# Optimization experiments

Measured on AMD Instinct MI355X. Metric: run time of the kernel, lower is better.

Reference implementation:

```python
import jax, jax.numpy as jnp
import numpy as np

N_IN, N_OUT, BATCH, LEVELS = 8192, 256, 1024, 2


def binarize(x):
    # clip + sign with straight-through gradient (Ioffe trick)
    c = jnp.clip(x, -1.0, 1.0)
    return c + jax.lax.stop_gradient(jnp.sign(c) - c)


def setup_inputs() -> dict:
    key = jax.random.key(0)
    ks = jax.random.split(key, 5)
    stdv = 1.0 / np.sqrt(N_IN)
    x = jax.random.normal(ks[0], (LEVELS, BATCH, N_IN), dtype=jnp.float32)
    w = jax.random.normal(ks[1], (32, N_IN, N_OUT), dtype=jnp.float32) * stdv
    gamma = jnp.ones((1,), dtype=jnp.float32)
    rand_map_0 = jax.random.randint(ks[2], (N_IN,), 0, N_IN, dtype=jnp.int32)
    rand_map_1 = jax.random.randint(ks[3], (N_IN,), 0, N_IN, dtype=jnp.int32)
    rand_map_2 = jax.random.randint(ks[4], (N_IN,), 0, N_IN, dtype=jnp.int32)
    pruning_mask = jnp.ones((N_IN, N_OUT), dtype=jnp.float32)
    return {"x": x, "w": w, "gamma": gamma, "pruning_mask": pruning_mask,
            "rand_map_0": rand_map_0, "rand_map_1": rand_map_1, "rand_map_2": rand_map_2}


def reference(x, w, gamma, pruning_mask, rand_map_0, rand_map_1, rand_map_2):
    # levels==2, LUT==True, BINARY==True path of binary_dense
    constraint_gamma = jnp.abs(gamma[0])
    cw = constraint_gamma * binarize(w)            # [32, n_in, n_out]
    mw = cw * pruning_mask[None, :, :]             # pruned clamped weights
    B, n_out = x.shape[1], mw.shape[2]
    out = jnp.zeros((B, n_out), dtype=x.dtype)
    for l in range(LEVELS):
        xl = x[l]                                   # [B, n_in] residual-binarization level l
        # original input + three random-map gathered shuffles
        streams = [xl, xl[:, rand_map_0], xl[:, rand_map_1], xl[:, rand_map_2]]
        # pos = (1+sign)/2*|x|, neg = (1-sign)/2*|x|  (one-hot sign selectors scaled by magnitude)
        pos = [(1.0 + binarize(s)) * 0.5 * jnp.abs(s) for s in streams]
        neg = [(1.0 - binarize(s)) * 0.5 * jnp.abs(s) for s in streams]
        for c in range(16):                         # truth table over 4 binary inputs
            bits = [(c >> (3 - i)) & 1 for i in range(4)]  # x is MSB, xs2 is LSB; 0->pos, 1->neg
            f = pos[0] if bits[0] == 0 else neg[0]
            for i in range(1, 4):
                f = f * (pos[i] if bits[i] == 0 else neg[i])
            out = out + f @ mw[16 * l + c]
    return out
```

## Files before the change

kernel.cpp:

```cpp
#include <hip/hip_runtime.h>
#include <hip/hip_fp16.h>


#define N_IN   8192
#define N_OUT  256
#define BATCH  1024
#define LEVELS 2

#define KSLICES 64
#define BTILES  4
#define BT      256
#define CHUNK_K 8
#define ROWP    264

__global__ __launch_bounds__(256) void pass_mc(const float* __restrict__ x,
                                               const int* __restrict__ rm0,
                                               const int* __restrict__ rm1,
                                               const int* __restrict__ rm2,
                                               unsigned int* __restrict__ mc) {
  __shared__ float xrow[N_IN];
  const int lb = blockIdx.x;
  const size_t base = (size_t)lb * N_IN;
  const float4* xv = (const float4*)(x + base);
  const int t = threadIdx.x;
#pragma unroll
  for (int j = 0; j < 8; ++j) {
    float4 v = xv[t + j * 256];
    *(float4*)&xrow[4 * (t + j * 256)] = v;
  }
  __syncthreads();
#pragma unroll 4
  for (int j = 0; j < 32; ++j) {
    const int k = t + j * 256;
    const int r0 = rm0[k], r1 = rm1[k], r2 = rm2[k];
    const float s0 = xrow[k], s1 = xrow[r0], s2 = xrow[r1], s3 = xrow[r2];
    const float m = fabsf(s0 * s1 * s2 * s3);
    const unsigned c = ((s0 < 0.f) ? 8u : 0u) | ((s1 < 0.f) ? 4u : 0u) |
                       ((s2 < 0.f) ? 2u : 0u) | ((s3 < 0.f) ? 1u : 0u);
    mc[base + k] = (__float_as_uint(m) & ~0xFu) | c;
  }
}

__global__ __launch_bounds__(512, 2) void main_fma(const float* __restrict__ w,
                                                   const float* __restrict__ mask,
                                                   const unsigned int* __restrict__ mc,
                                                   float* __restrict__ part) {
  __shared__ __half lw[4 * 16 * ROWP];
  __shared__ unsigned int lmc[LEVELS * CHUNK_K * 256];

  const int ks = blockIdx.x;
  const int bt = blockIdx.y;
  const int t = threadIdx.x;
  const int lane = t & 63;
  const int wid = t >> 6;
  const int wb = wid * 32;

  float acc[32][4];
#pragma unroll
  for (int i = 0; i < 32; ++i) {
    acc[i][0] = 0.f; acc[i][1] = 0.f; acc[i][2] = 0.f; acc[i][3] = 0.f;
  }

  const int s_ku = t >> 7;
  const int s_r  = (t >> 3) & 15;
  const int s_ob = (t & 7) * 32;

  for (int kc = 0; kc < 128 / CHUNK_K; ++kc) {
    const int k0 = ks * 128 + kc * CHUNK_K;
    __syncthreads();
    {
      const int l = t >> 8, b = t & 255;
      const unsigned int* src =
          mc + ((size_t)(l * BATCH + bt * BT + b) * N_IN + k0);
      const uint4 v0 = *(const uint4*)src;
      const uint4 v1 = *(const uint4*)(src + 4);
      unsigned int* dst = &lmc[l * (CHUNK_K * 256) + b];
      dst[0 * 256] = v0.x; dst[1 * 256] = v0.y; dst[2 * 256] = v0.z; dst[3 * 256] = v0.w;
      dst[4 * 256] = v1.x; dst[5 * 256] = v1.y; dst[6 * 256] = v1.z; dst[7 * 256] = v1.w;
    }
    __syncthreads();

    for (int sub = 0; sub < 4; ++sub) {
      if (sub) __syncthreads();
      {
        const int u = sub * 4 + s_ku;
        const int l = u >> 3, kk = u & 7;
        const int k = k0 + kk;
        const int row = l * 16 + s_r;
        const float* wsrc = w + ((size_t)(row * N_IN + k) * N_OUT + s_ob);
        const float* msrc = mask + ((size_t)k * N_OUT + s_ob);
        __half hbuf[32];
#pragma unroll
        for (int j = 0; j < 8; ++j) {
          const float4 wv = *(const float4*)(wsrc + j * 4);
          const float4 mv = *(const float4*)(msrc + j * 4);
          hbuf[4 * j + 0] = __float2half((wv.x > 0.f) ? mv.x : ((wv.x < 0.f) ? -mv.x : 0.f));
          hbuf[4 * j + 1] = __float2half((wv.y > 0.f) ? mv.y : ((wv.y < 0.f) ? -mv.y : 0.f));
          hbuf[4 * j + 2] = __float2half((wv.z > 0.f) ? mv.z : ((wv.z < 0.f) ? -mv.z : 0.f));
          hbuf[4 * j + 3] = __float2half((wv.w > 0.f) ? mv.w : ((wv.w < 0.f) ? -mv.w : 0.f));
        }
        __half* dst = &lw[s_ku * (16 * ROWP) + s_r * ROWP + s_ob];
#pragma unroll
        for (int j = 0; j < 4; ++j) *(uint4*)(dst + j * 8) = *(const uint4*)&hbuf[j * 8];
      }
      __syncthreads();

#pragma unroll
      for (int ul = 0; ul < 4; ++ul) {
        const int u = sub * 4 + ul;
        const int l = u >> 3, kk = u & 7;
        const unsigned int* mrow = &lmc[l * (CHUNK_K * 256) + kk * 256 + wb];
        const __half* wbase = &lw[ul * (16 * ROWP)];
#pragma unroll
        for (int i = 0; i < 32; i += 4) {
          const uint4 q = *(const uint4*)(mrow + i);
#define DO_B(UQ, AI)                                                        \
  {                                                                         \
    const unsigned uq = (UQ);                                               \
    const float m = __uint_as_float(uq & ~0xFu);                            \
    union { uint2 u2; __half2 h[2]; } wv_;                                  \
    wv_.u2 = *(const uint2*)(wbase + (uq & 0xFu) * ROWP + lane * 4);        \
    acc[AI][0] += m * __half2float(wv_.h[0].x);                             \
    acc[AI][1] += m * __half2float(wv_.h[0].y);                             \
    acc[AI][2] += m * __half2float(wv_.h[1].x);                             \
    acc[AI][3] += m * __half2float(wv_.h[1].y);                             \
  }
          DO_B(q.x, i + 0)
          DO_B(q.y, i + 1)
          DO_B(q.z, i + 2)
          DO_B(q.w, i + 3)
#undef DO_B
        }
      }
    }
  }

  float* dst = part + ((size_t)(ks * BATCH + bt * BT + wb) * N_OUT) + lane * 4;
#pragma unroll
  for (int i = 0; i < 32; ++i) *(float4*)(dst + (size_t)i * N_OUT) = *(const float4*)acc[i];
}

__global__ __launch_bounds__(256) void reduce_part(const float* __restrict__ part,
                                                   const float* __restrict__ gamma,
                                                   float* __restrict__ out) {
  const int b = blockIdx.x, o = threadIdx.x;
  const float g = fabsf(gamma[0]);
  const float* p = part + (size_t)b * N_OUT + o;
  float s = 0.f;
#pragma unroll
  for (int ks = 0; ks < KSLICES; ++ks) s += p[(size_t)ks * BATCH * N_OUT];
  out[b * N_OUT + o] = g * s;
}

extern "C" void kernel_launch(void* const* d_in, const int* in_sizes, int n_in,
                              void* d_out, int out_size, void* d_ws, size_t ws_size,
                              hipStream_t stream) {
  const float* x     = (const float*)d_in[0];
  const float* w     = (const float*)d_in[1];
  const float* gamma = (const float*)d_in[2];
  const float* mask  = (const float*)d_in[3];
  const int* rm0     = (const int*)d_in[4];
  const int* rm1     = (const int*)d_in[5];
  const int* rm2     = (const int*)d_in[6];
  float* out = (float*)d_out;

  unsigned int* mc = (unsigned int*)d_ws;
  float* part = (float*)((char*)d_ws + (size_t)LEVELS * BATCH * N_IN * 4);
  (void)in_sizes; (void)n_in; (void)out_size; (void)ws_size;

  pass_mc<<<dim3(LEVELS * BATCH), 256, 0, stream>>>(x, rm0, rm1, rm2, mc);
  main_fma<<<dim3(KSLICES, BTILES), 512, 0, stream>>>(w, mask, mc, part);
  reduce_part<<<dim3(BATCH), 256, 0, stream>>>(part, gamma, out);
}
```

Baseline: 1.020 ms.

## Prepack weights to 8-bit half-high bytes and atomically reduce into output

Adds a pre-pass that converts sign(w)*mask into one byte per weight (the high byte of the fp16 value), so main_fma streams a quarter of the weight bytes and expands them with byte-perm instructions. The batch tile is halved to 128 with 4 blocks per CU, which doubles the blocks and lowers register pressure but makes each block re-read the weights for fewer batch rows. The partial buffer and its reduction kernel are replaced by float atomicAdd into a zeroed output, followed by a gamma-scaling kernel. In exchange the packing pass reads the full fp32 weight tensor on every call, and the atomics make the summation order nondeterministic.

```diff
diff --git a/kernel.cpp b/kernel.cpp
--- a/kernel.cpp
+++ b/kernel.cpp
@@ -8,10 +8,38 @@
 #define LEVELS 2
 
 #define KSLICES 64
-#define BTILES  4
-#define BT      256
-#define CHUNK_K 8
-#define ROWP    264
+#define BTILES  8
+#define BT      128
+
+__global__ __launch_bounds__(256) void zero_out(float* __restrict__ out) {
+  out[blockIdx.x * 256 + threadIdx.x] = 0.f;
+}
+
+__global__ __launch_bounds__(256) void scale_out(float* __restrict__ out,
+                                                 const float* __restrict__ gamma) {
+  const int i = blockIdx.x * 256 + threadIdx.x;
+  out[i] *= fabsf(gamma[0]);
+}
+
+__global__ __launch_bounds__(256) void pass_w(const float* __restrict__ w,
+                                              const float* __restrict__ mask,
+                                              unsigned char* __restrict__ sw) {
+  const size_t base = ((size_t)blockIdx.x * 256 + threadIdx.x) * 8;
+  const size_t mo = base & (size_t)(N_IN * N_OUT - 1);
+  float wv[8], mv[8];
+  *(float4*)&wv[0] = *(const float4*)(w + base);
+  *(float4*)&wv[4] = *(const float4*)(w + base + 4);
+  *(float4*)&mv[0] = *(const float4*)(mask + mo);
+  *(float4*)&mv[4] = *(const float4*)(mask + mo + 4);
+  unsigned int u0 = 0, u1 = 0;
+#pragma unroll
+  for (int j = 0; j < 8; ++j) {
+    const float v = (wv[j] > 0.f) ? mv[j] : ((wv[j] < 0.f) ? -mv[j] : 0.f);
+    const unsigned int b = (unsigned int)(__half_as_ushort(__float2half(v)) >> 8);
+    if (j < 4) u0 |= b << (j * 8); else u1 |= b << ((j - 4) * 8);
+  }
+  *(uint2*)(sw + base) = make_uint2(u0, u1);
+}
 
 __global__ __launch_bounds__(256) void pass_mc(const float* __restrict__ x,
                                                const int* __restrict__ rm0,
@@ -41,89 +69,81 @@
   }
 }
 
-__global__ __launch_bounds__(512, 2) void main_fma(const float* __restrict__ w,
-                                                   const float* __restrict__ mask,
+__global__ __launch_bounds__(512, 4) void main_fma(const unsigned char* __restrict__ sw,
                                                    const unsigned int* __restrict__ mc,
-                                                   float* __restrict__ part) {
-  __shared__ __half lw[4 * 16 * ROWP];
-  __shared__ unsigned int lmc[LEVELS * CHUNK_K * 256];
+                                                   float* __restrict__ out) {
+  __shared__ __half lw[4 * 16 * 256];
+  __shared__ unsigned int lmc[16 * 128];
 
   const int ks = blockIdx.x;
   const int bt = blockIdx.y;
   const int t = threadIdx.x;
   const int lane = t & 63;
   const int wid = t >> 6;
-  const int wb = wid * 32;
+  const int wb = wid * 16;
 
-  float acc[32][4];
+  float acc[16][4];
 #pragma unroll
-  for (int i = 0; i < 32; ++i) {
-    acc[i][0] = 0.f; acc[i][1] = 0.f; acc[i][2] = 0.f; acc[i][3] = 0.f;
-  }
+  for (int i = 0; i < 16; ++i) { acc[i][0] = acc[i][1] = acc[i][2] = acc[i][3] = 0.f; }
 
-  const int s_ku = t >> 7;
-  const int s_r  = (t >> 3) & 15;
-  const int s_ob = (t & 7) * 32;
+  const int s_kul = t >> 7;
+  const int s_r   = (t >> 3) & 15;
+  const int s_ob  = (t & 7) * 32;
 
-  for (int kc = 0; kc < 128 / CHUNK_K; ++kc) {
-    const int k0 = ks * 128 + kc * CHUNK_K;
+  const int g_l = t >> 8;
+  const int g_b = (t >> 1) & 127;
+  const int g_h = t & 1;
+
+  for (int kc = 0; kc < 16; ++kc) {
+    const int k0 = ks * 128 + kc * 8;
     __syncthreads();
     {
-      const int l = t >> 8, b = t & 255;
-      const unsigned int* src =
-          mc + ((size_t)(l * BATCH + bt * BT + b) * N_IN + k0);
-      const uint4 v0 = *(const uint4*)src;
-      const uint4 v1 = *(const uint4*)(src + 4);
-      unsigned int* dst = &lmc[l * (CHUNK_K * 256) + b];
-      dst[0 * 256] = v0.x; dst[1 * 256] = v0.y; dst[2 * 256] = v0.z; dst[3 * 256] = v0.w;
-      dst[4 * 256] = v1.x; dst[5 * 256] = v1.y; dst[6 * 256] = v1.z; dst[7 * 256] = v1.w;
+      const uint4 v = *(const uint4*)(mc + ((size_t)(g_l * BATCH + bt * BT + g_b) * N_IN + k0 + g_h * 4));
+      unsigned int* dst = &lmc[(g_l * 8 + g_h * 4) * 128 + g_b];
+      dst[0 * 128] = v.x; dst[1 * 128] = v.y; dst[2 * 128] = v.z; dst[3 * 128] = v.w;
     }
     __syncthreads();
 
     for (int sub = 0; sub < 4; ++sub) {
       if (sub) __syncthreads();
       {
-        const int u = sub * 4 + s_ku;
-        const int l = u >> 3, kk = u & 7;
-        const int k = k0 + kk;
-        const int row = l * 16 + s_r;
-        const float* wsrc = w + ((size_t)(row * N_IN + k) * N_OUT + s_ob);
-        const float* msrc = mask + ((size_t)k * N_OUT + s_ob);
-        __half hbuf[32];
+        const int ku = sub * 4 + s_kul;
+        const int l = ku >> 3, kk = ku & 7;
+        const unsigned char* src =
+            sw + ((size_t)((l * 16 + s_r) * N_IN + (k0 + kk)) * N_OUT + s_ob);
+        const uint4 a = ((const uint4*)src)[0];
+        const uint4 b = ((const uint4*)src)[1];
+        unsigned int dec[16];
+        const unsigned int xs[8] = {a.x, a.y, a.z, a.w, b.x, b.y, b.z, b.w};
 #pragma unroll
         for (int j = 0; j < 8; ++j) {
-          const float4 wv = *(const float4*)(wsrc + j * 4);
-          const float4 mv = *(const float4*)(msrc + j * 4);
-          hbuf[4 * j + 0] = __float2half((wv.x > 0.f) ? mv.x : ((wv.x < 0.f) ? -mv.x : 0.f));
-          hbuf[4 * j + 1] = __float2half((wv.y > 0.f) ? mv.y : ((wv.y < 0.f) ? -mv.y : 0.f));
-          hbuf[4 * j + 2] = __float2half((wv.z > 0.f) ? mv.z : ((wv.z < 0.f) ? -mv.z : 0.f));
-          hbuf[4 * j + 3] = __float2half((wv.w > 0.f) ? mv.w : ((wv.w < 0.f) ? -mv.w : 0.f));
+          dec[2 * j + 0] = __builtin_amdgcn_perm(0u, xs[j], 0x01040004u);
+          dec[2 * j + 1] = __builtin_amdgcn_perm(0u, xs[j], 0x03040204u);
         }
-        __half* dst = &lw[s_ku * (16 * ROWP) + s_r * ROWP + s_ob];
+        unsigned int* dst = (unsigned int*)&lw[(s_kul * 16 + s_r) * 256 + s_ob];
 #pragma unroll
-        for (int j = 0; j < 4; ++j) *(uint4*)(dst + j * 8) = *(const uint4*)&hbuf[j * 8];
+        for (int j = 0; j < 4; ++j) *(uint4*)(dst + 4 * j) = *(const uint4*)&dec[4 * j];
       }
       __syncthreads();
 
 #pragma unroll
-      for (int ul = 0; ul < 4; ++ul) {
-        const int u = sub * 4 + ul;
-        const int l = u >> 3, kk = u & 7;
-        const unsigned int* mrow = &lmc[l * (CHUNK_K * 256) + kk * 256 + wb];
-        const __half* wbase = &lw[ul * (16 * ROWP)];
+      for (int kul = 0; kul < 4; ++kul) {
+        const int ku = sub * 4 + kul;
+        const unsigned int* mrow = &lmc[ku * 128 + wb];
+        const __half* wsel = lw + kul * 4096 + lane * 4;
 #pragma unroll
-        for (int i = 0; i < 32; i += 4) {
+        for (int i = 0; i < 16; i += 4) {
           const uint4 q = *(const uint4*)(mrow + i);
-#define DO_B(UQ, AI)                                                        \
-  {                                                                         \
-    const unsigned uq = (UQ);                                               \
-    const float m = __uint_as_float(uq & ~0xFu);                            \
-    union { uint2 u2; __half2 h[2]; } wv_;                                  \
-    wv_.u2 = *(const uint2*)(wbase + (uq & 0xFu) * ROWP + lane * 4);        \
-    acc[AI][0] += m * __half2float(wv_.h[0].x);                             \
-    acc[AI][1] += m * __half2float(wv_.h[0].y);                             \
-    acc[AI][2] += m * __half2float(wv_.h[1].x);                             \
-    acc[AI][3] += m * __half2float(wv_.h[1].y);                             \
+#define DO_B(UQ, AI)                                                      \
+  {                                                                       \
+    const unsigned uq = (UQ);                                             \
+    const float m = __uint_as_float(uq & 0xFFFFFFF0u);                    \
+    union { uint2 u; __half h[4]; } wv_;                                  \
+    wv_.u = *(const uint2*)(wsel + ((uq & 15u) << 8));                    \
+    acc[AI][0] = fmaf(m, __half2float(wv_.h[0]), acc[AI][0]);             \
+    acc[AI][1] = fmaf(m, __half2float(wv_.h[1]), acc[AI][1]);             \
+    acc[AI][2] = fmaf(m, __half2float(wv_.h[2]), acc[AI][2]);             \
+    acc[AI][3] = fmaf(m, __half2float(wv_.h[3]), acc[AI][3]);             \
   }
           DO_B(q.x, i + 0)
           DO_B(q.y, i + 1)
@@ -135,21 +155,15 @@
     }
   }
 
-  float* dst = part + ((size_t)(ks * BATCH + bt * BT + wb) * N_OUT) + lane * 4;
+  float* dst0 = out + (size_t)(bt * BT + wb) * N_OUT + lane * 4;
 #pragma unroll
-  for (int i = 0; i < 32; ++i) *(float4*)(dst + (size_t)i * N_OUT) = *(const float4*)acc[i];
-}
-
-__global__ __launch_bounds__(256) void reduce_part(const float* __restrict__ part,
-                                                   const float* __restrict__ gamma,
-                                                   float* __restrict__ out) {
-  const int b = blockIdx.x, o = threadIdx.x;
-  const float g = fabsf(gamma[0]);
-  const float* p = part + (size_t)b * N_OUT + o;
-  float s = 0.f;
-#pragma unroll
-  for (int ks = 0; ks < KSLICES; ++ks) s += p[(size_t)ks * BATCH * N_OUT];
-  out[b * N_OUT + o] = g * s;
+  for (int i = 0; i < 16; ++i) {
+    float* d = dst0 + (size_t)i * N_OUT;
+    atomicAdd(d + 0, acc[i][0]);
+    atomicAdd(d + 1, acc[i][1]);
+    atomicAdd(d + 2, acc[i][2]);
+    atomicAdd(d + 3, acc[i][3]);
+  }
 }
 
 extern "C" void kernel_launch(void* const* d_in, const int* in_sizes, int n_in,
@@ -165,10 +179,12 @@
   float* out = (float*)d_out;
 
   unsigned int* mc = (unsigned int*)d_ws;
-  float* part = (float*)((char*)d_ws + (size_t)LEVELS * BATCH * N_IN * 4);
+  unsigned char* sw = (unsigned char*)d_ws + (size_t)LEVELS * BATCH * N_IN * 4;
   (void)in_sizes; (void)n_in; (void)out_size; (void)ws_size;
 
+  zero_out<<<dim3(BATCH), 256, 0, stream>>>(out);
+  pass_w<<<dim3(32 * N_IN * N_OUT / (256 * 8)), 256, 0, stream>>>(w, mask, sw);
   pass_mc<<<dim3(LEVELS * BATCH), 256, 0, stream>>>(x, rm0, rm1, rm2, mc);
-  main_fma<<<dim3(KSLICES, BTILES), 512, 0, stream>>>(w, mask, mc, part);
-  reduce_part<<<dim3(BATCH), 256, 0, stream>>>(part, gamma, out);
+  main_fma<<<dim3(KSLICES, BTILES), 512, 0, stream>>>(sw, mc, out);
+  scale_out<<<dim3(BATCH), 256, 0, stream>>>(out, gamma);
 }
```

Result: no change. 1.037 ms (+1.7%).
